# Kernel tuning notes

Hardware: AMD Instinct MI355X
Metric: run time of the kernel (lower is better)

The kernel has to match this reference:

```python
import jax, jax.numpy as jnp
import numpy as np

N, E, D, H1, H2 = 50000, 800000, 128, 128, 128


def setup_inputs() -> dict:
    key = jax.random.key(0)
    ks = jax.random.split(key, 9)
    s = 0.05
    return {
        "x": jax.random.normal(ks[0], (N, D), dtype=jnp.float32),
        "edge_index": jax.random.randint(ks[1], (2, E), 0, N, dtype=jnp.int64),
        "W_l1": jax.random.normal(ks[2], (D, H1), dtype=jnp.float32) * s,
        "b_l1": jnp.zeros((H1,), dtype=jnp.float32),
        "W_r1": jax.random.normal(ks[3], (D, H1), dtype=jnp.float32) * s,
        "W_l2": jax.random.normal(ks[4], (H1, H2), dtype=jnp.float32) * s,
        "b_l2": jnp.zeros((H2,), dtype=jnp.float32),
        "W_r2": jax.random.normal(ks[5], (H1, H2), dtype=jnp.float32) * s,
        "W_e": jax.random.normal(ks[6], (2 * H2, 1), dtype=jnp.float32) * s,
        "b_e": jnp.zeros((1,), dtype=jnp.float32),
    }


def _sage_conv(h, src, tgt, n_nodes, W_l, b_l, W_r):
    # PyG SAGEConv (mean aggr): out = lin_l(mean_{j in N(i)} h_j) + lin_r(h_i)
    msg = h[src]                                              # [E, F] gather
    agg = jax.ops.segment_sum(msg, tgt, num_segments=n_nodes)  # [N, F]
    cnt = jax.ops.segment_sum(jnp.ones((src.shape[0], 1), h.dtype), tgt,
                              num_segments=n_nodes)            # [N, 1]
    mean = agg / jnp.maximum(cnt, 1.0)                         # empty nbrs -> 0
    return mean @ W_l + b_l + h @ W_r


def reference(x, edge_index, W_l1, b_l1, W_r1, W_l2, b_l2, W_r2, W_e, b_e):
    src, tgt = edge_index[0], edge_index[1]
    n_nodes = x.shape[0]
    h = jax.nn.relu(_sage_conv(x, src, tgt, n_nodes, W_l1, b_l1, W_r1))
    # dropout is identity in eval mode
    h = _sage_conv(h, src, tgt, n_nodes, W_l2, b_l2, W_r2)
    z = jnp.concatenate([h[src], h[tgt]], axis=-1)  # [E, 2*H2]
    y = z @ W_e + b_e                                # [E, 1]
    return jax.nn.sigmoid(y)
```

## Files before the change

### kernel.cpp

```cpp
#include <hip/hip_runtime.h>

#define NN 50000
#define NE 800000
#define DD 128
#define BUCKETS 196
#define PB 4096
#define PBLK 196
#define EMAX 6144
#define BPAD 264
#define PACKB 3125
#define WTB 128

typedef unsigned int uint_t;
typedef unsigned short ush_t;
typedef __attribute__((ext_vector_type(8))) short short8;
typedef __attribute__((ext_vector_type(4))) float f32x4;

__device__ __forceinline__ float bflo(uint_t u) { return __uint_as_float(u << 16); }
__device__ __forceinline__ float bfhi(uint_t u) { return __uint_as_float(u & 0xffff0000u); }
__device__ __forceinline__ ush_t f2bf(float f) {
  uint_t u = __float_as_uint(f);
  u += 0x7fffu + ((u >> 16) & 1u);
  return (ush_t)(u >> 16);
}
__device__ __forceinline__ uint_t pack2(float a, float b) {
  return (uint_t)f2bf(a) | ((uint_t)f2bf(b) << 16);
}

__device__ __forceinline__ int ld_idx(const void* ei, int is64, long long i) {
  return is64 ? (int)((const long long*)ei)[i] : ((const int*)ei)[i];
}

__device__ __forceinline__ int detect64(const void* ei) {
  const unsigned long long* p = (const unsigned long long*)ei;
  unsigned long long w = p[threadIdx.x & 63];
  return __ballot((w >> 32) != 0) == 0ull ? 1 : 0;
}

__device__ __forceinline__ int block_incl_scan(int v, int tid, int* wsum) {
  int lane = tid & 63, wave = tid >> 6;
  int s = v;
#pragma unroll
  for (int off = 1; off < 64; off <<= 1) {
    int u = __shfl_up(s, off, 64);
    if (lane >= off) s += u;
  }
  if (lane == 63) wsum[wave] = s;
  __syncthreads();
  int base = 0;
  if (wave > 0) base += wsum[0];
  if (wave > 1) base += wsum[1];
  if (wave > 2) base += wsum[2];
  return base + s;
}

__global__ __launch_bounds__(256) void prep_part_k(
    const void* __restrict__ ei, int* __restrict__ bcur,
    uint_t* __restrict__ pbuf, uint_t* __restrict__ epk,
    const float* __restrict__ x, ush_t* __restrict__ xbc,
    const float* __restrict__ Wl1, const float* __restrict__ Wr1,
    const float* __restrict__ Wl2, const float* __restrict__ Wr2,
    const float* __restrict__ We, const float* __restrict__ bl2,
    const float* __restrict__ be,
    ush_t* __restrict__ Wt1, float* __restrict__ uv, float* __restrict__ cc) {
  __shared__ int hist[256];
  __shared__ int basel[256];
  __shared__ int cur[256];
  __shared__ int gbase[256];
  __shared__ int wsum[4];
  __shared__ uint_t buf[PB];
  __shared__ unsigned char bbuf[PB];
  int tid = threadIdx.x;
  int blk = blockIdx.x;
  if (blk >= PBLK) {
    int blk2 = blk - PBLK;
    if (blk2 < 2) {
      const float* W = blk2 ? Wr2 : Wl2;
      int base = blk2 * 256;
      int wave = tid >> 6, lane = tid & 63;
      float e0 = We[lane], e1 = We[64 + lane];
      float f0 = We[128 + lane], f1 = We[192 + lane];
      for (int k = wave * 32; k < wave * 32 + 32; ++k) {
        float m0 = W[k * DD + lane];
        float m1 = W[k * DD + 64 + lane];
        float p = m0 * e0 + m1 * e1;
        float q = m0 * f0 + m1 * f1;
#pragma unroll
        for (int off = 32; off > 0; off >>= 1) {
          p += __shfl_down(p, off, 64);
          q += __shfl_down(q, off, 64);
        }
        if (lane == 0) {
          uv[base + k] = p;
          uv[base + 128 + k] = q;
        }
      }
      return;
    }
    if (blk2 == 2) {
      if (tid < 64) {
        int k = tid;
        float p = bl2[k] * (We[k] + We[128 + k]) +
                  bl2[k + 64] * (We[k + 64] + We[192 + k]);
#pragma unroll
        for (int off = 32; off > 0; off >>= 1) p += __shfl_down(p, off, 64);
        if (k == 0) cc[0] = p + be[0];
      }
      return;
    }
    blk2 -= 3;
    if (blk2 < PACKB) {
      int i = blk2 * 256 + tid;
      int node = i >> 4;
      int g = i & 15;
      const float4* xp = reinterpret_cast<const float4*>(x) + (size_t)i * 2;
      float4 v0 = xp[0];
      float4 v1 = xp[1];
      uint4 o;
      o.x = pack2(v0.x, v0.y);
      o.y = pack2(v0.z, v0.w);
      o.z = pack2(v1.x, v1.y);
      o.w = pack2(v1.z, v1.w);
      int chunk = g >> 1;
      int l8 = (g & 1) * 8;
      *reinterpret_cast<uint4*>(xbc + ((size_t)chunk * NN + node) * 16 + l8) = o;
      return;
    }
    blk2 -= PACKB;
    int e = blk2 * 256 + tid;
    int col = e >> 8;
    int k = e & 255;
    float v = (k < DD) ? Wl1[k * DD + col] : Wr1[(k - DD) * DD + col];
    Wt1[col * 256 + k] = f2bf(v);
    return;
  }
  int is64 = detect64(ei);
  hist[tid] = 0;
  __syncthreads();
  long long base = (long long)blk * PB;
  uint_t pv[PB / 256];
#pragma unroll
  for (int i = 0; i < PB / 256; ++i) {
    long long e = base + i * 256 + tid;
    if (e < NE) {
      int s = ld_idx(ei, is64, e);
      int d = ld_idx(ei, is64, (long long)NE + e);
      pv[i] = ((uint_t)(d >> 8) << 24) | ((uint_t)(d & 255) << 16) | (uint_t)s;
      epk[e] = ((uint_t)d << 16) | (uint_t)s;
      atomicAdd(&hist[d >> 8], 1);
    } else {
      pv[i] = 0xFFFFFFFFu;
    }
  }
  __syncthreads();
  int hv = hist[tid];
  int incl = block_incl_scan(hv, tid, wsum);
  basel[tid] = incl - hv;
  cur[tid] = incl - hv;
  if (hv > 0) gbase[tid] = atomicAdd(&bcur[tid], hv);
  __syncthreads();
#pragma unroll
  for (int i = 0; i < PB / 256; ++i) {
    uint_t p = pv[i];
    if (p != 0xFFFFFFFFu) {
      int b = p >> 24;
      int r = atomicAdd(&cur[b], 1);
      buf[r] = p & 0xFFFFFFu;
      bbuf[r] = (unsigned char)b;
    }
  }
  __syncthreads();
  int total = basel[255] + hist[255];
  for (int j = tid; j < total; j += 256) {
    int b = bbuf[j];
    int slot = gbase[b] + (j - basel[b]);
    if (slot < EMAX) pbuf[(size_t)b * EMAX + slot] = buf[j];
  }
}

__global__ __launch_bounds__(256) void csr_k(const uint_t* __restrict__ pbuf,
                                             const int* __restrict__ bcur,
                                             int* __restrict__ offsets,
                                             ush_t* __restrict__ srclist) {
  __shared__ int cnt[256];
  __shared__ int scur[256];
  __shared__ int wsum[4];
  __shared__ int sgb, scnt, stot;
  __shared__ uint_t ebuf[EMAX];
  int tid = threadIdx.x;
  int b = blockIdx.x;
  int v = 0;
  if (tid < BUCKETS) {
    v = bcur[tid];
    if (v > EMAX) v = EMAX;
  }
  int incl = block_incl_scan(v, tid, wsum);
  if (tid == b) { sgb = incl - v; scnt = v; }
  if (tid == BUCKETS - 1) stot = incl;
  cnt[tid] = 0;
  __syncthreads();
  int gb = sgb;
  int ecnt = scnt;
  for (int j = tid; j < ecnt; j += 256) {
    uint_t e = pbuf[(size_t)b * EMAX + j];
    ebuf[j] = e;
    atomicAdd(&cnt[(e >> 16) & 255], 1);
  }
  __syncthreads();
  int c = cnt[tid];
  int incl2 = block_incl_scan(c, tid, wsum);
  int ex = incl2 - c;
  scur[tid] = ex;
  int node = b * 256 + tid;
  if (node < NN) offsets[node] = gb + ex;
  if (b == BUCKETS - 1 && tid == 0) offsets[NN] = stot;
  __syncthreads();
  for (int j = tid; j < ecnt; j += 256) {
    uint_t e = ebuf[j];
    int p = atomicAdd(&scur[(e >> 16) & 255], 1);
    srclist[gb + p] = (ush_t)(e & 0xFFFFu);
  }
}

__global__ __launch_bounds__(256) void agg_k(const ush_t* __restrict__ xbc,
                                             const ush_t* __restrict__ srclist,
                                             const int* __restrict__ offsets,
                                             ush_t* __restrict__ meanb) {
  int bid = blockIdx.x;
  int chunk = bid & 7;
  int grp = bid >> 3;
  int tid = threadIdx.x;
  int node = grp * 128 + (tid >> 1);
  if (node >= NN) return;
  int half = tid & 1;
  const ush_t* base = xbc + (size_t)chunk * NN * 16 + half * 8;
  int beg = offsets[node];
  int end = offsets[node + 1];
  float a0 = 0.f, a1 = 0.f, a2 = 0.f, a3 = 0.f;
  float a4 = 0.f, a5 = 0.f, a6 = 0.f, a7 = 0.f;
  int e = beg;
  for (; e + 4 <= end; e += 4) {
    int s0 = srclist[e];
    int s1 = srclist[e + 1];
    int s2 = srclist[e + 2];
    int s3 = srclist[e + 3];
    uint4 v0 = *reinterpret_cast<const uint4*>(base + (size_t)s0 * 16);
    uint4 v1 = *reinterpret_cast<const uint4*>(base + (size_t)s1 * 16);
    uint4 v2 = *reinterpret_cast<const uint4*>(base + (size_t)s2 * 16);
    uint4 v3 = *reinterpret_cast<const uint4*>(base + (size_t)s3 * 16);
    a0 += bflo(v0.x); a1 += bfhi(v0.x); a2 += bflo(v0.y); a3 += bfhi(v0.y);
    a4 += bflo(v0.z); a5 += bfhi(v0.z); a6 += bflo(v0.w); a7 += bfhi(v0.w);
    a0 += bflo(v1.x); a1 += bfhi(v1.x); a2 += bflo(v1.y); a3 += bfhi(v1.y);
    a4 += bflo(v1.z); a5 += bfhi(v1.z); a6 += bflo(v1.w); a7 += bfhi(v1.w);
    a0 += bflo(v2.x); a1 += bfhi(v2.x); a2 += bflo(v2.y); a3 += bfhi(v2.y);
    a4 += bflo(v2.z); a5 += bfhi(v2.z); a6 += bflo(v2.w); a7 += bfhi(v2.w);
    a0 += bflo(v3.x); a1 += bfhi(v3.x); a2 += bflo(v3.y); a3 += bfhi(v3.y);
    a4 += bflo(v3.z); a5 += bfhi(v3.z); a6 += bflo(v3.w); a7 += bfhi(v3.w);
  }
  for (; e < end; ++e) {
    int s = srclist[e];
    uint4 v = *reinterpret_cast<const uint4*>(base + (size_t)s * 16);
    a0 += bflo(v.x); a1 += bfhi(v.x); a2 += bflo(v.y); a3 += bfhi(v.y);
    a4 += bflo(v.z); a5 += bfhi(v.z); a6 += bflo(v.w); a7 += bfhi(v.w);
  }
  float inv = 1.0f / fmaxf((float)(end - beg), 1.0f);
  uint4 o;
  o.x = pack2(a0 * inv, a1 * inv);
  o.y = pack2(a2 * inv, a3 * inv);
  o.z = pack2(a4 * inv, a5 * inv);
  o.w = pack2(a6 * inv, a7 * inv);
  *reinterpret_cast<uint4*>(meanb + (size_t)node * DD + chunk * 16 + half * 8) = o;
}

__global__ __launch_bounds__(256, 2) void sage_l1(
    const ush_t* __restrict__ meanb, const ush_t* __restrict__ xbc,
    const ush_t* __restrict__ Wt1, const float* __restrict__ bl,
    const float* __restrict__ uv, float2* __restrict__ t12,
    float2* __restrict__ r12) {
  __shared__ ush_t sB[128 * BPAD];
  int tid = threadIdx.x;
  int lane = tid & 63;
  int wave = tid >> 6;
  int n15 = lane & 15, quad = lane >> 4;
  int nb = blockIdx.x * 64;
#pragma unroll
  for (int it = 0; it < 16; ++it) {
    int i = it * 256 + tid;
    int col = i >> 5, c = i & 31;
    *reinterpret_cast<short8*>(&sB[col * BPAD + c * 8]) =
        reinterpret_cast<const short8*>(Wt1)[i];
  }
  __syncthreads();
  int row = nb + wave * 16 + n15;
  int arow = (row < NN) ? row : (NN - 1);
  const ush_t* a0 = meanb + (size_t)arow * DD;
  f32x4 acc[8];
#pragma unroll
  for (int t = 0; t < 8; ++t) acc[t] = (f32x4){0.f, 0.f, 0.f, 0.f};
#pragma unroll
  for (int c = 0; c < 8; ++c) {
    short8 af;
    if (c < 4) {
      af = *reinterpret_cast<const short8*>(a0 + c * 32 + quad * 8);
    } else {
      int fb = (c - 4) * 32 + quad * 8;
      af = *reinterpret_cast<const short8*>(
          xbc + ((size_t)(fb >> 4) * NN + arow) * 16 + (fb & 15));
    }
    int kb = c * 32 + quad * 8;
#pragma unroll
    for (int t = 0; t < 8; ++t) {
      short8 bf = *reinterpret_cast<const short8*>(&sB[(t * 16 + n15) * BPAD + kb]);
      acc[t] = __builtin_amdgcn_mfma_f32_16x16x32_bf16(af, bf, acc[t], 0, 0, 0);
    }
  }
  float p1[4] = {0.f, 0.f, 0.f, 0.f};
  float p2[4] = {0.f, 0.f, 0.f, 0.f};
  float q1[4] = {0.f, 0.f, 0.f, 0.f};
  float q2[4] = {0.f, 0.f, 0.f, 0.f};
#pragma unroll
  for (int t = 0; t < 8; ++t) {
    int col = t * 16 + n15;
    float b = bl[col];
    float U1 = uv[col];
    float U2 = uv[128 + col];
    float V1 = uv[256 + col];
    float V2 = uv[384 + col];
#pragma unroll
    for (int reg = 0; reg < 4; ++reg) {
      float h = fmaxf(acc[t][reg] + b, 0.f);
      p1[reg] += h * U1;
      p2[reg] += h * U2;
      q1[reg] += h * V1;
      q2[reg] += h * V2;
    }
  }
#pragma unroll
  for (int reg = 0; reg < 4; ++reg) {
    float a1 = p1[reg], a2 = p2[reg], b1 = q1[reg], b2 = q2[reg];
    for (int off = 8; off > 0; off >>= 1) {
      a1 += __shfl_down(a1, off, 16);
      a2 += __shfl_down(a2, off, 16);
      b1 += __shfl_down(b1, off, 16);
      b2 += __shfl_down(b2, off, 16);
    }
    int r = nb + wave * 16 + quad * 4 + reg;
    if (n15 == 0 && r < NN) {
      t12[r] = make_float2(a1, a2);
      r12[r] = make_float2(b1, b2);
    }
  }
}

__global__ __launch_bounds__(256) void agg2s_k(const float2* __restrict__ t12,
                                               const ush_t* __restrict__ srclist,
                                               const int* __restrict__ offsets,
                                               const float2* __restrict__ r12,
                                               float2* __restrict__ s12) {
  int t = blockIdx.x * 256 + threadIdx.x;
  int node = t >> 4;
  int lane = t & 15;
  int beg = offsets[node];
  int end = offsets[node + 1];
  float sx = 0.f, sy = 0.f;
  for (int c = beg + lane; c < end; c += 16) {
    int s = srclist[c];
    float2 v = t12[s];
    sx += v.x;
    sy += v.y;
  }
  for (int off = 8; off > 0; off >>= 1) {
    sx += __shfl_down(sx, off, 16);
    sy += __shfl_down(sy, off, 16);
  }
  if (lane == 0) {
    float inv = 1.0f / fmaxf((float)(end - beg), 1.0f);
    float2 r = r12[node];
    s12[node] = make_float2(sx * inv + r.x, sy * inv + r.y);
  }
}

__global__ __launch_bounds__(256) void edge_k(const uint_t* __restrict__ epk,
                                              const float2* __restrict__ s12,
                                              const float* __restrict__ cc,
                                              float* __restrict__ out) {
  int e = blockIdx.x * 256 + threadIdx.x;
  uint_t p = epk[e];
  float2 a = s12[p & 0xFFFFu];
  float2 b = s12[p >> 16];
  float v = a.x + b.y + cc[0];
  out[e] = 1.0f / (1.0f + __expf(-v));
}

extern "C" void kernel_launch(void* const* d_in, const int* in_sizes, int n_in,
                              void* d_out, int out_size, void* d_ws, size_t ws_size,
                              hipStream_t stream) {
  const float* x   = (const float*)d_in[0];
  const void*  ei  = d_in[1];
  const float* Wl1 = (const float*)d_in[2];
  const float* bl1 = (const float*)d_in[3];
  const float* Wr1 = (const float*)d_in[4];
  const float* Wl2 = (const float*)d_in[5];
  const float* bl2 = (const float*)d_in[6];
  const float* Wr2 = (const float*)d_in[7];
  const float* We  = (const float*)d_in[8];
  const float* be  = (const float*)d_in[9];
  float* out = (float*)d_out;

  int* bcur       = (int*)d_ws;
  int* offsets    = bcur + 256;
  uint_t* epk     = (uint_t*)(offsets + 50004);
  uint_t* pbuf    = epk + NE;
  ush_t* srclist  = (ush_t*)(pbuf + (size_t)BUCKETS * EMAX);
  ush_t* xbc      = srclist + NE;
  ush_t* meanb    = xbc + (size_t)NN * DD;
  float2* t12     = (float2*)(meanb + (size_t)NN * DD);
  float2* r12     = t12 + NN;
  float2* s12     = r12 + NN;
  ush_t* Wt1      = (ush_t*)(s12 + NN);
  float* uv       = (float*)(Wt1 + 32768);
  float* cc       = uv + 512;

  hipMemsetAsync(bcur, 0, 256 * sizeof(int), stream);
  prep_part_k<<<PBLK + 3 + PACKB + WTB, 256, 0, stream>>>(
      ei, bcur, pbuf, epk, x, xbc, Wl1, Wr1, Wl2, Wr2, We, bl2, be, Wt1, uv, cc);
  csr_k<<<BUCKETS, 256, 0, stream>>>(pbuf, bcur, offsets, srclist);

  agg_k<<<((NN + 127) / 128) * 8, 256, 0, stream>>>(xbc, srclist, offsets, meanb);

  sage_l1<<<(NN + 63) / 64, 256, 0, stream>>>(meanb, xbc, Wt1, bl1, uv, t12, r12);

  agg2s_k<<<(NN * 16) / 256, 256, 0, stream>>>(t12, srclist, offsets, r12, s12);

  edge_k<<<NE / 256, 256, 0, stream>>>(epk, s12, cc, out);
}
```

Baseline: 190.9 us.

## Widen feature chunks to 32 and cooperatively load neighbor indices via shuffles

Changes the packed bf16 feature layout from 8 chunks of 16 features to 4 chunks of 32 features, so each neighbor gather reads a 64-byte contiguous segment with four threads per node. The aggregation loop now has the four lanes of a node load 16 source indices cooperatively and broadcast them with shuffles, then issue 16 independent gathers per iteration. The goal is fewer redundant index loads and more memory-level parallelism. The cost is higher register use (16 uint4 per thread) and wasted lanes on nodes with few neighbors.

```diff
diff --git a/kernel.cpp b/kernel.cpp
--- a/kernel.cpp
+++ b/kernel.cpp
@@ -121,9 +121,9 @@
       o.y = pack2(v0.z, v0.w);
       o.z = pack2(v1.x, v1.y);
       o.w = pack2(v1.z, v1.w);
-      int chunk = g >> 1;
-      int l8 = (g & 1) * 8;
-      *reinterpret_cast<uint4*>(xbc + ((size_t)chunk * NN + node) * 16 + l8) = o;
+      int chunk = g >> 2;
+      int off32 = (g & 3) * 8;
+      *reinterpret_cast<uint4*>(xbc + ((size_t)chunk * NN + node) * 32 + off32) = o;
       return;
     }
     blk2 -= PACKB;
@@ -227,41 +227,48 @@
                                              const int* __restrict__ offsets,
                                              ush_t* __restrict__ meanb) {
   int bid = blockIdx.x;
-  int chunk = bid & 7;
-  int grp = bid >> 3;
+  int chunk = bid & 3;
+  int grp = bid >> 2;
   int tid = threadIdx.x;
-  int node = grp * 128 + (tid >> 1);
+  int node = grp * 64 + (tid >> 2);
   if (node >= NN) return;
-  int half = tid & 1;
-  const ush_t* base = xbc + (size_t)chunk * NN * 16 + half * 8;
+  int l4 = tid & 3;
+  int lane = tid & 63;
+  int lb = lane & 60;
+  const ush_t* base = xbc + (size_t)chunk * NN * 32 + l4 * 8;
   int beg = offsets[node];
   int end = offsets[node + 1];
   float a0 = 0.f, a1 = 0.f, a2 = 0.f, a3 = 0.f;
   float a4 = 0.f, a5 = 0.f, a6 = 0.f, a7 = 0.f;
-  int e = beg;
-  for (; e + 4 <= end; e += 4) {
-    int s0 = srclist[e];
-    int s1 = srclist[e + 1];
-    int s2 = srclist[e + 2];
-    int s3 = srclist[e + 3];
-    uint4 v0 = *reinterpret_cast<const uint4*>(base + (size_t)s0 * 16);
-    uint4 v1 = *reinterpret_cast<const uint4*>(base + (size_t)s1 * 16);
-    uint4 v2 = *reinterpret_cast<const uint4*>(base + (size_t)s2 * 16);
-    uint4 v3 = *reinterpret_cast<const uint4*>(base + (size_t)s3 * 16);
-    a0 += bflo(v0.x); a1 += bfhi(v0.x); a2 += bflo(v0.y); a3 += bfhi(v0.y);
-    a4 += bflo(v0.z); a5 += bfhi(v0.z); a6 += bflo(v0.w); a7 += bfhi(v0.w);
-    a0 += bflo(v1.x); a1 += bfhi(v1.x); a2 += bflo(v1.y); a3 += bfhi(v1.y);
-    a4 += bflo(v1.z); a5 += bfhi(v1.z); a6 += bflo(v1.w); a7 += bfhi(v1.w);
-    a0 += bflo(v2.x); a1 += bfhi(v2.x); a2 += bflo(v2.y); a3 += bfhi(v2.y);
-    a4 += bflo(v2.z); a5 += bfhi(v2.z); a6 += bflo(v2.w); a7 += bfhi(v2.w);
-    a0 += bflo(v3.x); a1 += bfhi(v3.x); a2 += bflo(v3.y); a3 += bfhi(v3.y);
-    a4 += bflo(v3.z); a5 += bfhi(v3.z); a6 += bflo(v3.w); a7 += bfhi(v3.w);
-  }
-  for (; e < end; ++e) {
-    int s = srclist[e];
-    uint4 v = *reinterpret_cast<const uint4*>(base + (size_t)s * 16);
-    a0 += bflo(v.x); a1 += bfhi(v.x); a2 += bflo(v.y); a3 += bfhi(v.y);
-    a4 += bflo(v.z); a5 += bfhi(v.z); a6 += bflo(v.w); a7 += bfhi(v.w);
+  for (int c = beg; c < end; c += 16) {
+    int m = end - c;
+    int i0 = c + l4, i1 = c + 4 + l4, i2 = c + 8 + l4, i3 = c + 12 + l4;
+    int s0 = (i0 < end) ? (int)srclist[i0] : 0;
+    int s1 = (i1 < end) ? (int)srclist[i1] : 0;
+    int s2 = (i2 < end) ? (int)srclist[i2] : 0;
+    int s3 = (i3 < end) ? (int)srclist[i3] : 0;
+    uint4 v[16];
+#pragma unroll
+    for (int j = 0; j < 4; ++j)
+      v[j] = *reinterpret_cast<const uint4*>(base + (size_t)__shfl(s0, lb + j, 64) * 32);
+#pragma unroll
+    for (int j = 0; j < 4; ++j)
+      v[4 + j] = *reinterpret_cast<const uint4*>(base + (size_t)__shfl(s1, lb + j, 64) * 32);
+#pragma unroll
+    for (int j = 0; j < 4; ++j)
+      v[8 + j] = *reinterpret_cast<const uint4*>(base + (size_t)__shfl(s2, lb + j, 64) * 32);
+#pragma unroll
+    for (int j = 0; j < 4; ++j)
+      v[12 + j] = *reinterpret_cast<const uint4*>(base + (size_t)__shfl(s3, lb + j, 64) * 32);
+#pragma unroll
+    for (int j = 0; j < 16; ++j) {
+      if (j < m) {
+        a0 += bflo(v[j].x); a1 += bfhi(v[j].x);
+        a2 += bflo(v[j].y); a3 += bfhi(v[j].y);
+        a4 += bflo(v[j].z); a5 += bfhi(v[j].z);
+        a6 += bflo(v[j].w); a7 += bfhi(v[j].w);
+      }
+    }
   }
   float inv = 1.0f / fmaxf((float)(end - beg), 1.0f);
   uint4 o;
@@ -269,7 +276,7 @@
   o.y = pack2(a2 * inv, a3 * inv);
   o.z = pack2(a4 * inv, a5 * inv);
   o.w = pack2(a6 * inv, a7 * inv);
-  *reinterpret_cast<uint4*>(meanb + (size_t)node * DD + chunk * 16 + half * 8) = o;
+  *reinterpret_cast<uint4*>(meanb + (size_t)node * DD + chunk * 32 + l4 * 8) = o;
 }
 
 __global__ __launch_bounds__(256, 2) void sage_l1(
@@ -303,9 +310,8 @@
     if (c < 4) {
       af = *reinterpret_cast<const short8*>(a0 + c * 32 + quad * 8);
     } else {
-      int fb = (c - 4) * 32 + quad * 8;
       af = *reinterpret_cast<const short8*>(
-          xbc + ((size_t)(fb >> 4) * NN + arow) * 16 + (fb & 15));
+          xbc + ((size_t)(c - 4) * NN + arow) * 32 + quad * 8);
     }
     int kb = c * 32 + quad * 8;
 #pragma unroll
@@ -426,7 +432,7 @@
       ei, bcur, pbuf, epk, x, xbc, Wl1, Wr1, Wl2, Wr2, We, bl2, be, Wt1, uv, cc);
   csr_k<<<BUCKETS, 256, 0, stream>>>(pbuf, bcur, offsets, srclist);
 
-  agg_k<<<((NN + 127) / 128) * 8, 256, 0, stream>>>(xbc, srclist, offsets, meanb);
+  agg_k<<<((NN + 63) / 64) * 4, 256, 0, stream>>>(xbc, srclist, offsets, meanb);
 
   sage_l1<<<(NN + 63) / 64, 256, 0, stream>>>(meanb, xbc, Wt1, bl1, uv, t12, r12);
 
```

After: 182.4 us. 4.4% less time.
